# Optimization experiments

Hardware: AMD Instinct MI355X
Metric: run time of the kernel (lower is better)

The kernel has to match this reference:

```python
import jax, jax.numpy as jnp
import numpy as np

# module hyperparameters (from init_kwargs)
STRIDE, PAD, DIL = 1, 1, 1
GROUPS, DG = 1, 1
KH, KW = 3, 3
CIN, COUT = 256, 256


def _mdcn_forward(x, offset, mask, weight, bias):
    B, C, H, W = x.shape
    Cout = weight.shape[0]
    K = KH * KW
    Ho = (H + 2 * PAD - (DIL * (KH - 1) + 1)) // STRIDE + 1
    Wo = (W + 2 * PAD - (DIL * (KW - 1) + 1)) // STRIDE + 1
    Cg = C // DG

    # offset channel layout: ((g*K + k)*2 + {0: dy, 1: dx})
    off = offset.reshape(B, DG, KH, KW, 2, Ho, Wo)
    base_y = (jnp.arange(Ho) * STRIDE - PAD)[None, :] + DIL * jnp.arange(KH)[:, None]  # [KH,Ho]
    base_x = (jnp.arange(Wo) * STRIDE - PAD)[None, :] + DIL * jnp.arange(KW)[:, None]  # [KW,Wo]
    sy = base_y[None, None, :, None, :, None].astype(x.dtype) + off[:, :, :, :, 0]  # [B,DG,KH,KW,Ho,Wo]
    sx = base_x[None, None, None, :, None, :].astype(x.dtype) + off[:, :, :, :, 1]

    y0f = jnp.floor(sy); x0f = jnp.floor(sx)
    wy = sy - y0f; wx = sx - x0f
    y0 = y0f.astype(jnp.int32); x0 = x0f.astype(jnp.int32)

    xg = x.reshape(B, DG, Cg, H * W)

    def corner(yc, xc, w):
        valid = (yc >= 0) & (yc < H) & (xc >= 0) & (xc < W)
        idx = jnp.clip(yc, 0, H - 1) * W + jnp.clip(xc, 0, W - 1)  # [B,DG,KH,KW,Ho,Wo]
        v = jnp.take_along_axis(xg, idx.reshape(B, DG, 1, -1), axis=3)  # [B,DG,Cg,K*Ho*Wo]
        v = v.reshape(B, DG, Cg, KH, KW, Ho, Wo)
        return v * (w * valid.astype(x.dtype))[:, :, None]

    val = (corner(y0, x0, (1 - wy) * (1 - wx))
           + corner(y0, x0 + 1, (1 - wy) * wx)
           + corner(y0 + 1, x0, wy * (1 - wx))
           + corner(y0 + 1, x0 + 1, wy * wx))  # [B,DG,Cg,KH,KW,Ho,Wo]

    cols = val * mask.reshape(B, DG, 1, KH, KW, Ho, Wo)
    cols = cols.reshape(B, GROUPS, (C // GROUPS) * K, Ho * Wo)
    wg = weight.reshape(GROUPS, Cout // GROUPS, (C // GROUPS) * K)
    out = jnp.einsum('gok,bgkp->bgop', wg, cols).reshape(B, Cout, Ho, Wo)
    return out + bias[None, :, None, None]


def setup_inputs() -> dict:
    key = jax.random.key(0)
    k1, k2, k3, k4 = jax.random.split(key, 4)
    B, H, W = 4, 64, 64
    x = jax.random.normal(k1, (B, CIN, H, W), dtype=jnp.float32)
    offset = jax.random.normal(k2, (B, 2 * DG * KH * KW, H, W), dtype=jnp.float32)
    mask = jax.random.uniform(k3, (B, DG * KH * KW, H, W), dtype=jnp.float32)
    stdv = 1.0 / np.sqrt(CIN * KH * KW)
    weight = jax.random.uniform(k4, (COUT, CIN // GROUPS, KH, KW), dtype=jnp.float32,
                                minval=-stdv, maxval=stdv)
    bias = jnp.zeros((COUT,), dtype=jnp.float32)
    return {"x": x, "offset": offset, "mask": mask, "weight": weight, "bias": bias}


def reference(x, offset, mask, weight, bias):
    return _mdcn_forward(x, offset, mask, weight, bias)
```

## Files before the change

kernel.cpp:

```cpp
#include <hip/hip_runtime.h>
#include <hip/hip_bf16.h>
#include <stdint.h>

#define KDIM 2304

typedef __bf16 bf16_t;
typedef bf16_t bf16x8 __attribute__((ext_vector_type(8)));
typedef float f32x4 __attribute__((ext_vector_type(4)));
typedef float f32x2 __attribute__((ext_vector_type(2)));

__device__ __forceinline__ float b2f_lo(uint32_t u) {
  union { uint32_t i; float f; } c; c.i = u << 16; return c.f;
}
__device__ __forceinline__ float b2f_hi(uint32_t u) {
  union { uint32_t i; float f; } c; c.i = u & 0xffff0000u; return c.f;
}
__device__ __forceinline__ uint32_t pk_bf16(float a, float b) {
  __hip_bfloat162 h = __float22bfloat162_rn(make_float2(a, b));
  union { __hip_bfloat162 h; uint32_t u; } c; c.h = h; return c.u;
}

__global__ __launch_bounds__(256) void k_prep(const float* __restrict__ x,
                                              uint16_t* __restrict__ xt,
                                              const float* __restrict__ w,
                                              uint16_t* __restrict__ wt2) {
  int tid = threadIdx.x;
  if (blockIdx.x < 2048) {
    __shared__ float tile[32][65];
    int b = blockIdx.x >> 9;
    int cgrp = (blockIdx.x >> 6) & 7;
    int sgrp = blockIdx.x & 63;
    int c0 = cgrp << 5, s0 = sgrp << 6;
#pragma unroll
    for (int it = 0; it < 2; ++it) {
      int f = tid + it * 256;
      int rr = f >> 4, col = (f & 15) << 2;
      float4 v = *(const float4*)&x[((size_t)(b * 256 + c0 + rr)) * 4096 + s0 + col];
      tile[rr][col + 0] = v.x;
      tile[rr][col + 1] = v.y;
      tile[rr][col + 2] = v.z;
      tile[rr][col + 3] = v.w;
    }
    __syncthreads();
    int sp = tid >> 2, cg = tid & 3;
    uint4 o;
    o.x = pk_bf16(tile[cg * 8 + 0][sp], tile[cg * 8 + 1][sp]);
    o.y = pk_bf16(tile[cg * 8 + 2][sp], tile[cg * 8 + 3][sp]);
    o.z = pk_bf16(tile[cg * 8 + 4][sp], tile[cg * 8 + 5][sp]);
    o.w = pk_bf16(tile[cg * 8 + 6][sp], tile[cg * 8 + 7][sp]);
    *(uint4*)&xt[((size_t)b * 4096 + s0 + sp) * 256 + c0 + cg * 8] = o;
  } else {
    __shared__ float wl[2304];
    int row = blockIdx.x - 2048;
    const float* wrow = w + (size_t)row * KDIM;
    for (int i2 = tid; i2 < 2304; i2 += 256) wl[i2] = wrow[i2];
    __syncthreads();
    int strip = row >> 4, r16 = row & 15;
    for (int c = tid; c < 288; c += 256) {
      int tap = c >> 5, rem = c & 31;
      int w64 = rem >> 3, kh = (rem >> 2) & 1, seg = rem & 3;
      int i = tap * 4 + w64;
      int cin0 = w64 * 64 + kh * 32 + seg * 8;
      int lanex = seg * 16 + r16;
      uint16_t* dst = wt2 + (size_t)i * 16384 + (size_t)(strip * 128 + kh * 64 + lanex) * 8;
      uint4 o;
      o.x = pk_bf16(wl[(cin0 + 0) * 9 + tap], wl[(cin0 + 1) * 9 + tap]);
      o.y = pk_bf16(wl[(cin0 + 2) * 9 + tap], wl[(cin0 + 3) * 9 + tap]);
      o.z = pk_bf16(wl[(cin0 + 4) * 9 + tap], wl[(cin0 + 5) * 9 + tap]);
      o.w = pk_bf16(wl[(cin0 + 6) * 9 + tap], wl[(cin0 + 7) * 9 + tap]);
      *(uint4*)dst = o;
    }
  }
}

__device__ __forceinline__ void mk_corners(int tap, int p, int ho,
                                           const float* s_off, const float* s_msk,
                                           float cw[4], int cpo[4]) {
  int kh = tap / 3, kw = tap - kh * 3;
  float dy = s_off[(2 * tap) * 64 + p];
  float dx = s_off[(2 * tap + 1) * 64 + p];
  float mm = s_msk[tap * 64 + p];
  float sy = (float)(ho - 1 + kh) + dy;
  float sx = (float)(p - 1 + kw) + dx;
  float fy = floorf(sy), fx = floorf(sx);
  int y0 = (int)fy, x0 = (int)fx;
  float wy = sy - fy, wx = sx - fx;
#pragma unroll
  for (int cy = 0; cy < 2; ++cy) {
#pragma unroll
    for (int cx = 0; cx < 2; ++cx) {
      int y = y0 + cy, xx = x0 + cx;
      float wgt = (cy ? wy : 1.f - wy) * (cx ? wx : 1.f - wx) * mm;
      bool v = ((unsigned)y < 64u) && ((unsigned)xx < 64u);
      wgt = v ? wgt : 0.f;
      int yc = min(max(y, 0), 63), xc = min(max(xx, 0), 63);
      cw[cy * 2 + cx] = wgt;
      cpo[cy * 2 + cx] = ((yc << 6) + xc) * 256;
    }
  }
}

__global__ __launch_bounds__(512, 4) void k_fused(const uint16_t* __restrict__ xt,
                                                  const uint16_t* __restrict__ wt2,
                                                  const float* __restrict__ off,
                                                  const float* __restrict__ msk,
                                                  const float* __restrict__ bias,
                                                  float* __restrict__ out) {
  __shared__ __align__(16) uint16_t Bs[2][64][64];
  __shared__ float s_off[18 * 64];
  __shared__ float s_msk[9 * 64];

  int tid = threadIdx.x;
  int swz = ((int)blockIdx.x & 7) * 64 + ((int)blockIdx.x >> 3);
  int b = swz >> 7, ho = (swz >> 1) & 63, mh = swz & 1;

  const float* offb = off + (size_t)b * 18 * 4096 + ho * 64;
  for (int i = tid; i < 18 * 64; i += 512)
    s_off[i] = offb[(size_t)(i >> 6) * 4096 + (i & 63)];
  const float* mskb = msk + (size_t)b * 9 * 4096 + ho * 64;
  for (int i = tid; i < 9 * 64; i += 512)
    s_msk[i] = mskb[(size_t)(i >> 6) * 4096 + (i & 63)];

  int lane = tid & 63, wv = tid >> 6;
  int wm = wv >> 1, wn = wv & 1;
  int q = lane >> 4, r = lane & 15;
  int p = tid >> 3, cgh = tid & 7;
  const uint16_t* xtb = xt + (size_t)b * 1048576 + cgh * 8;
  int bcol = (cgh ^ (p & 7)) << 3;
  int awb = (mh * 4 + wm) * 2048;

  f32x4 acc[2][2];
#pragma unroll
  for (int mi = 0; mi < 2; ++mi)
#pragma unroll
    for (int ni = 0; ni < 2; ++ni) acc[mi][ni] = f32x4{0.f, 0.f, 0.f, 0.f};

  __syncthreads();

  float cw[4];
  int cpo[4];
  uint4 dnv[4];
  bf16x8 AFA[2][2], AFB[2][2];

  int c0 = (q ^ (r & 7)) << 3;
  int c1 = c0 ^ 32;
  int rb0 = (wn * 32 + r) * 64;

  mk_corners(0, p, ho, s_off, s_msk, cw, cpo);
#pragma unroll
  for (int c = 0; c < 4; ++c) dnv[c] = *(const uint4*)(xtb + cpo[c]);
  {
    const uint16_t* wp = wt2 + awb + lane * 8;
    AFA[0][0] = *(const bf16x8*)(wp);
    AFA[0][1] = *(const bf16x8*)(wp + 512);
    AFA[1][0] = *(const bf16x8*)(wp + 1024);
    AFA[1][1] = *(const bf16x8*)(wp + 1536);
  }
  {
    f32x2 f0 = {0.f, 0.f}, f1 = {0.f, 0.f}, f2 = {0.f, 0.f}, f3 = {0.f, 0.f};
#pragma unroll
    for (int c = 0; c < 4; ++c) {
      f32x2 wc = {cw[c], cw[c]};
      f0 += wc * f32x2{b2f_lo(dnv[c].x), b2f_hi(dnv[c].x)};
      f1 += wc * f32x2{b2f_lo(dnv[c].y), b2f_hi(dnv[c].y)};
      f2 += wc * f32x2{b2f_lo(dnv[c].z), b2f_hi(dnv[c].z)};
      f3 += wc * f32x2{b2f_lo(dnv[c].w), b2f_hi(dnv[c].w)};
    }
    uint4 o;
    o.x = pk_bf16(f0.x, f0.y);
    o.y = pk_bf16(f1.x, f1.y);
    o.z = pk_bf16(f2.x, f2.y);
    o.w = pk_bf16(f3.x, f3.y);
    *(uint4*)&Bs[0][p][bcol] = o;
  }
  __syncthreads();

#define BODY(I, AFC, AFN, DOMK, DODNV, DOAF, DOBL)                              \
  {                                                                             \
    if (DOMK) mk_corners(((I) + 1) >> 2, p, ho, s_off, s_msk, cw, cpo);         \
    if (DODNV) {                                                                \
      const int chw = (((I) + 1) & 3) << 6;                                     \
      dnv[0] = *(const uint4*)(xtb + cpo[0] + chw);                             \
      dnv[1] = *(const uint4*)(xtb + cpo[1] + chw);                             \
      dnv[2] = *(const uint4*)(xtb + cpo[2] + chw);                             \
      dnv[3] = *(const uint4*)(xtb + cpo[3] + chw);                             \
    }                                                                           \
    if (DOAF) {                                                                 \
      const uint16_t* wp = wt2 + (size_t)((I) + 1) * 16384 + awb + lane * 8;    \
      AFN[0][0] = *(const bf16x8*)(wp);                                         \
      AFN[0][1] = *(const bf16x8*)(wp + 512);                                   \
      AFN[1][0] = *(const bf16x8*)(wp + 1024);                                  \
      AFN[1][1] = *(const bf16x8*)(wp + 1536);                                  \
    }                                                                           \
    {                                                                           \
      const uint16_t* bsrow = &Bs[(I) & 1][0][0];                               \
      bf16x8 b00 = *(const bf16x8*)(bsrow + rb0 + c0);           \
      bf16x8 b01 = *(const bf16x8*)(bsrow + rb0 + c1);           \
      bf16x8 b10 = *(const bf16x8*)(bsrow + rb0 + 1024 + c0);    \
      bf16x8 b11 = *(const bf16x8*)(bsrow + rb0 + 1024 + c1);    \
      __builtin_amdgcn_s_setprio(1);                                            \
      acc[0][0] = __builtin_amdgcn_mfma_f32_16x16x32_bf16(AFC[0][0], b00, acc[0][0], 0, 0, 0); \
      acc[0][1] = __builtin_amdgcn_mfma_f32_16x16x32_bf16(AFC[0][0], b10, acc[0][1], 0, 0, 0); \
      acc[1][0] = __builtin_amdgcn_mfma_f32_16x16x32_bf16(AFC[1][0], b00, acc[1][0], 0, 0, 0); \
      acc[1][1] = __builtin_amdgcn_mfma_f32_16x16x32_bf16(AFC[1][0], b10, acc[1][1], 0, 0, 0); \
      acc[0][0] = __builtin_amdgcn_mfma_f32_16x16x32_bf16(AFC[0][1], b01, acc[0][0], 0, 0, 0); \
      acc[0][1] = __builtin_amdgcn_mfma_f32_16x16x32_bf16(AFC[0][1], b11, acc[0][1], 0, 0, 0); \
      acc[1][0] = __builtin_amdgcn_mfma_f32_16x16x32_bf16(AFC[1][1], b01, acc[1][0], 0, 0, 0); \
      acc[1][1] = __builtin_amdgcn_mfma_f32_16x16x32_bf16(AFC[1][1], b11, acc[1][1], 0, 0, 0); \
      __builtin_amdgcn_s_setprio(0);                                            \
    }                                                                           \
    if (DOBL) {                                                                 \
      f32x2 f0 = {0.f, 0.f}, f1 = {0.f, 0.f}, f2 = {0.f, 0.f}, f3 = {0.f, 0.f};\
      _Pragma("unroll")                                                         \
      for (int c = 0; c < 4; ++c) {                                             \
        f32x2 wc = {cw[c], cw[c]};                                              \
        f0 += wc * f32x2{b2f_lo(dnv[c].x), b2f_hi(dnv[c].x)};                   \
        f1 += wc * f32x2{b2f_lo(dnv[c].y), b2f_hi(dnv[c].y)};                   \
        f2 += wc * f32x2{b2f_lo(dnv[c].z), b2f_hi(dnv[c].z)};                   \
        f3 += wc * f32x2{b2f_lo(dnv[c].w), b2f_hi(dnv[c].w)};                   \
      }                                                                         \
      uint4 o;                                                                  \
      o.x = pk_bf16(f0.x, f0.y);                                                \
      o.y = pk_bf16(f1.x, f1.y);                                                \
      o.z = pk_bf16(f2.x, f2.y);                                                \
      o.w = pk_bf16(f3.x, f3.y);                                                \
      *(uint4*)&Bs[((I) + 1) & 1][p][bcol] = o;                                 \
    }                                                                           \
    __syncthreads();                                                            \
  }

#pragma unroll 1
  for (int ii = 0; ii < 8; ++ii) {
    int i0 = 4 * ii;
    BODY(i0 + 0, AFA, AFB, 0, 1, 1, 1)
    BODY(i0 + 1, AFB, AFA, 0, 1, 1, 1)
    BODY(i0 + 2, AFA, AFB, 0, 1, 1, 1)
    BODY(i0 + 3, AFB, AFA, 1, 1, 1, 1)
  }
  BODY(32, AFA, AFB, 0, 1, 1, 1)
  BODY(33, AFB, AFA, 0, 1, 1, 1)
  BODY(34, AFA, AFB, 0, 1, 1, 1)
  BODY(35, AFB, AFA, 0, 0, 0, 0)
#undef BODY

#pragma unroll
  for (int mi = 0; mi < 2; ++mi) {
#pragma unroll
    for (int j = 0; j < 4; ++j) {
      int m = mh * 128 + wm * 32 + mi * 16 + q * 4 + j;
      float bv = bias[m];
#pragma unroll
      for (int ni = 0; ni < 2; ++ni) {
        int wog = wn * 32 + ni * 16 + r;
        out[((size_t)(b * 256 + m)) * 4096 + ho * 64 + wog] = acc[mi][ni][j] + bv;
      }
    }
  }
}

extern "C" void kernel_launch(void* const* d_in, const int* in_sizes, int n_in,
                              void* d_out, int out_size, void* d_ws, size_t ws_size,
                              hipStream_t stream) {
  (void)in_sizes; (void)n_in; (void)out_size; (void)ws_size;
  const float* x      = (const float*)d_in[0];
  const float* offset = (const float*)d_in[1];
  const float* mask   = (const float*)d_in[2];
  const float* weight = (const float*)d_in[3];
  const float* bias   = (const float*)d_in[4];
  float* out = (float*)d_out;

  uint8_t* ws = (uint8_t*)d_ws;
  uint16_t* xt  = (uint16_t*)ws;
  uint16_t* wt2 = (uint16_t*)(ws + 8388608);

  k_prep<<<dim3(2304), 256, 0, stream>>>(x, xt, weight, wt2);
  k_fused<<<dim3(512), 512, 0, stream>>>(xt, wt2, offset, mask, bias, out);
}
```

Before: 128.5 us.

## Compute all 256 output channels per block and double the K step

Each block now covers the full 256-wide output-channel dimension with 1024 threads, instead of two blocks each covering half. The bilinear-sampled column tile is therefore gathered once per output row rather than twice. Each iteration now consumes 128 K-elements, which halves the iteration and barrier count. In exchange, weight fragments are loaded in the same iteration that uses them instead of being prefetched one step ahead, so global load latency is exposed before the MFMAs. The grid also shrinks to 256 large blocks, which limits occupancy options.

```diff
diff --git a/kernel.cpp b/kernel.cpp
--- a/kernel.cpp
+++ b/kernel.cpp
@@ -100,34 +100,34 @@
   }
 }
 
-__global__ __launch_bounds__(512, 4) void k_fused(const uint16_t* __restrict__ xt,
-                                                  const uint16_t* __restrict__ wt2,
-                                                  const float* __restrict__ off,
-                                                  const float* __restrict__ msk,
-                                                  const float* __restrict__ bias,
-                                                  float* __restrict__ out) {
-  __shared__ __align__(16) uint16_t Bs[2][64][64];
+__global__ __launch_bounds__(1024, 4) void k_fused(const uint16_t* __restrict__ xt,
+                                                   const uint16_t* __restrict__ wt2,
+                                                   const float* __restrict__ off,
+                                                   const float* __restrict__ msk,
+                                                   const float* __restrict__ bias,
+                                                   float* __restrict__ out) {
+  __shared__ __align__(16) uint16_t Bs[2][64][128];
   __shared__ float s_off[18 * 64];
   __shared__ float s_msk[9 * 64];
 
   int tid = threadIdx.x;
-  int swz = ((int)blockIdx.x & 7) * 64 + ((int)blockIdx.x >> 3);
-  int b = swz >> 7, ho = (swz >> 1) & 63, mh = swz & 1;
+  int swz = ((int)blockIdx.x & 7) * 32 + ((int)blockIdx.x >> 3);
+  int b = swz >> 6, ho = swz & 63;
 
   const float* offb = off + (size_t)b * 18 * 4096 + ho * 64;
-  for (int i = tid; i < 18 * 64; i += 512)
+  for (int i = tid; i < 18 * 64; i += 1024)
     s_off[i] = offb[(size_t)(i >> 6) * 4096 + (i & 63)];
   const float* mskb = msk + (size_t)b * 9 * 4096 + ho * 64;
-  for (int i = tid; i < 9 * 64; i += 512)
+  for (int i = tid; i < 9 * 64; i += 1024)
     s_msk[i] = mskb[(size_t)(i >> 6) * 4096 + (i & 63)];
 
   int lane = tid & 63, wv = tid >> 6;
   int wm = wv >> 1, wn = wv & 1;
   int q = lane >> 4, r = lane & 15;
-  int p = tid >> 3, cgh = tid & 7;
-  const uint16_t* xtb = xt + (size_t)b * 1048576 + cgh * 8;
-  int bcol = (cgh ^ (p & 7)) << 3;
-  int awb = (mh * 4 + wm) * 2048;
+  int p = tid >> 4, cg16 = tid & 15;
+  int half = cg16 >> 3, cg = cg16 & 7;
+  const uint16_t* xtb = xt + (size_t)b * 1048576 + cg * 8;
+  int wcol = (((half << 3) | (cg ^ (p & 7))) << 3);
 
   f32x4 acc[2][2];
 #pragma unroll
@@ -140,21 +140,17 @@
   float cw[4];
   int cpo[4];
   uint4 dnv[4];
-  bf16x8 AFA[2][2], AFB[2][2];
+  bf16x8 AF0[2][2], AF1[2][2];
 
   int c0 = (q ^ (r & 7)) << 3;
   int c1 = c0 ^ 32;
-  int rb0 = (wn * 32 + r) * 64;
+  int rowb0 = (wn * 32 + r) * 128;
 
   mk_corners(0, p, ho, s_off, s_msk, cw, cpo);
-#pragma unroll
-  for (int c = 0; c < 4; ++c) dnv[c] = *(const uint4*)(xtb + cpo[c]);
   {
-    const uint16_t* wp = wt2 + awb + lane * 8;
-    AFA[0][0] = *(const bf16x8*)(wp);
-    AFA[0][1] = *(const bf16x8*)(wp + 512);
-    AFA[1][0] = *(const bf16x8*)(wp + 1024);
-    AFA[1][1] = *(const bf16x8*)(wp + 1536);
+    const int chw = half << 6;
+#pragma unroll
+    for (int c = 0; c < 4; ++c) dnv[c] = *(const uint4*)(xtb + cpo[c] + chw);
   }
   {
     f32x2 f0 = {0.f, 0.f}, f1 = {0.f, 0.f}, f2 = {0.f, 0.f}, f3 = {0.f, 0.f};
@@ -171,42 +167,58 @@
     o.y = pk_bf16(f1.x, f1.y);
     o.z = pk_bf16(f2.x, f2.y);
     o.w = pk_bf16(f3.x, f3.y);
-    *(uint4*)&Bs[0][p][bcol] = o;
+    *(uint4*)&Bs[0][p][wcol] = o;
   }
   __syncthreads();
 
-#define BODY(I, AFC, AFN, DOMK, DODNV, DOAF, DOBL)                              \
+#define BODY(I, DOMK, DODNV, DOAF, DOBL)                                        \
   {                                                                             \
-    if (DOMK) mk_corners(((I) + 1) >> 2, p, ho, s_off, s_msk, cw, cpo);         \
+    if (DOMK) mk_corners(((I) + 1) >> 1, p, ho, s_off, s_msk, cw, cpo);         \
     if (DODNV) {                                                                \
-      const int chw = (((I) + 1) & 3) << 6;                                     \
+      const int chw = (((2 * ((I) + 1)) + half) & 3) << 6;                      \
       dnv[0] = *(const uint4*)(xtb + cpo[0] + chw);                             \
       dnv[1] = *(const uint4*)(xtb + cpo[1] + chw);                             \
       dnv[2] = *(const uint4*)(xtb + cpo[2] + chw);                             \
       dnv[3] = *(const uint4*)(xtb + cpo[3] + chw);                             \
     }                                                                           \
     if (DOAF) {                                                                 \
-      const uint16_t* wp = wt2 + (size_t)((I) + 1) * 16384 + awb + lane * 8;    \
-      AFN[0][0] = *(const bf16x8*)(wp);                                         \
-      AFN[0][1] = *(const bf16x8*)(wp + 512);                                   \
-      AFN[1][0] = *(const bf16x8*)(wp + 1024);                                  \
-      AFN[1][1] = *(const bf16x8*)(wp + 1536);                                  \
+      const uint16_t* wp = wt2 + (size_t)(2 * (I)) * 16384 + wm * 2048 + lane * 8; \
+      AF0[0][0] = *(const bf16x8*)(wp);                                         \
+      AF0[0][1] = *(const bf16x8*)(wp + 512);                                   \
+      AF0[1][0] = *(const bf16x8*)(wp + 1024);                                  \
+      AF0[1][1] = *(const bf16x8*)(wp + 1536);                                  \
+      AF1[0][0] = *(const bf16x8*)(wp + 16384);                                 \
+      AF1[0][1] = *(const bf16x8*)(wp + 16384 + 512);                           \
+      AF1[1][0] = *(const bf16x8*)(wp + 16384 + 1024);                          \
+      AF1[1][1] = *(const bf16x8*)(wp + 16384 + 1536);                          \
     }                                                                           \
     {                                                                           \
       const uint16_t* bsrow = &Bs[(I) & 1][0][0];                               \
-      bf16x8 b00 = *(const bf16x8*)(bsrow + rb0 + c0);           \
-      bf16x8 b01 = *(const bf16x8*)(bsrow + rb0 + c1);           \
-      bf16x8 b10 = *(const bf16x8*)(bsrow + rb0 + 1024 + c0);    \
-      bf16x8 b11 = *(const bf16x8*)(bsrow + rb0 + 1024 + c1);    \
+      bf16x8 bh0n0k0 = *(const bf16x8*)(bsrow + rowb0 + c0);                    \
+      bf16x8 bh0n0k1 = *(const bf16x8*)(bsrow + rowb0 + c1);                    \
+      bf16x8 bh0n1k0 = *(const bf16x8*)(bsrow + rowb0 + 2048 + c0);             \
+      bf16x8 bh0n1k1 = *(const bf16x8*)(bsrow + rowb0 + 2048 + c1);             \
+      bf16x8 bh1n0k0 = *(const bf16x8*)(bsrow + rowb0 + 64 + c0);               \
+      bf16x8 bh1n0k1 = *(const bf16x8*)(bsrow + rowb0 + 64 + c1);               \
+      bf16x8 bh1n1k0 = *(const bf16x8*)(bsrow + rowb0 + 2048 + 64 + c0);        \
+      bf16x8 bh1n1k1 = *(const bf16x8*)(bsrow + rowb0 + 2048 + 64 + c1);        \
       __builtin_amdgcn_s_setprio(1);                                            \
-      acc[0][0] = __builtin_amdgcn_mfma_f32_16x16x32_bf16(AFC[0][0], b00, acc[0][0], 0, 0, 0); \
-      acc[0][1] = __builtin_amdgcn_mfma_f32_16x16x32_bf16(AFC[0][0], b10, acc[0][1], 0, 0, 0); \
-      acc[1][0] = __builtin_amdgcn_mfma_f32_16x16x32_bf16(AFC[1][0], b00, acc[1][0], 0, 0, 0); \
-      acc[1][1] = __builtin_amdgcn_mfma_f32_16x16x32_bf16(AFC[1][0], b10, acc[1][1], 0, 0, 0); \
-      acc[0][0] = __builtin_amdgcn_mfma_f32_16x16x32_bf16(AFC[0][1], b01, acc[0][0], 0, 0, 0); \
-      acc[0][1] = __builtin_amdgcn_mfma_f32_16x16x32_bf16(AFC[0][1], b11, acc[0][1], 0, 0, 0); \
-      acc[1][0] = __builtin_amdgcn_mfma_f32_16x16x32_bf16(AFC[1][1], b01, acc[1][0], 0, 0, 0); \
-      acc[1][1] = __builtin_amdgcn_mfma_f32_16x16x32_bf16(AFC[1][1], b11, acc[1][1], 0, 0, 0); \
+      acc[0][0] = __builtin_amdgcn_mfma_f32_16x16x32_bf16(AF0[0][0], bh0n0k0, acc[0][0], 0, 0, 0); \
+      acc[0][1] = __builtin_amdgcn_mfma_f32_16x16x32_bf16(AF0[0][0], bh0n1k0, acc[0][1], 0, 0, 0); \
+      acc[1][0] = __builtin_amdgcn_mfma_f32_16x16x32_bf16(AF0[1][0], bh0n0k0, acc[1][0], 0, 0, 0); \
+      acc[1][1] = __builtin_amdgcn_mfma_f32_16x16x32_bf16(AF0[1][0], bh0n1k0, acc[1][1], 0, 0, 0); \
+      acc[0][0] = __builtin_amdgcn_mfma_f32_16x16x32_bf16(AF0[0][1], bh0n0k1, acc[0][0], 0, 0, 0); \
+      acc[0][1] = __builtin_amdgcn_mfma_f32_16x16x32_bf16(AF0[0][1], bh0n1k1, acc[0][1], 0, 0, 0); \
+      acc[1][0] = __builtin_amdgcn_mfma_f32_16x16x32_bf16(AF0[1][1], bh0n0k1, acc[1][0], 0, 0, 0); \
+      acc[1][1] = __builtin_amdgcn_mfma_f32_16x16x32_bf16(AF0[1][1], bh0n1k1, acc[1][1], 0, 0, 0); \
+      acc[0][0] = __builtin_amdgcn_mfma_f32_16x16x32_bf16(AF1[0][0], bh1n0k0, acc[0][0], 0, 0, 0); \
+      acc[0][1] = __builtin_amdgcn_mfma_f32_16x16x32_bf16(AF1[0][0], bh1n1k0, acc[0][1], 0, 0, 0); \
+      acc[1][0] = __builtin_amdgcn_mfma_f32_16x16x32_bf16(AF1[1][0], bh1n0k0, acc[1][0], 0, 0, 0); \
+      acc[1][1] = __builtin_amdgcn_mfma_f32_16x16x32_bf16(AF1[1][0], bh1n1k0, acc[1][1], 0, 0, 0); \
+      acc[0][0] = __builtin_amdgcn_mfma_f32_16x16x32_bf16(AF1[0][1], bh1n0k1, acc[0][0], 0, 0, 0); \
+      acc[0][1] = __builtin_amdgcn_mfma_f32_16x16x32_bf16(AF1[0][1], bh1n1k1, acc[0][1], 0, 0, 0); \
+      acc[1][0] = __builtin_amdgcn_mfma_f32_16x16x32_bf16(AF1[1][1], bh1n0k1, acc[1][0], 0, 0, 0); \
+      acc[1][1] = __builtin_amdgcn_mfma_f32_16x16x32_bf16(AF1[1][1], bh1n1k1, acc[1][1], 0, 0, 0); \
       __builtin_amdgcn_s_setprio(0);                                            \
     }                                                                           \
     if (DOBL) {                                                                 \
@@ -224,30 +236,25 @@
       o.y = pk_bf16(f1.x, f1.y);                                                \
       o.z = pk_bf16(f2.x, f2.y);                                                \
       o.w = pk_bf16(f3.x, f3.y);                                                \
-      *(uint4*)&Bs[((I) + 1) & 1][p][bcol] = o;                                 \
+      *(uint4*)&Bs[((I) + 1) & 1][p][wcol] = o;                                 \
     }                                                                           \
     __syncthreads();                                                            \
   }
 
 #pragma unroll 1
   for (int ii = 0; ii < 8; ++ii) {
-    int i0 = 4 * ii;
-    BODY(i0 + 0, AFA, AFB, 0, 1, 1, 1)
-    BODY(i0 + 1, AFB, AFA, 0, 1, 1, 1)
-    BODY(i0 + 2, AFA, AFB, 0, 1, 1, 1)
-    BODY(i0 + 3, AFB, AFA, 1, 1, 1, 1)
-  }
-  BODY(32, AFA, AFB, 0, 1, 1, 1)
-  BODY(33, AFB, AFA, 0, 1, 1, 1)
-  BODY(34, AFA, AFB, 0, 1, 1, 1)
-  BODY(35, AFB, AFA, 0, 0, 0, 0)
+    BODY(2 * ii + 0, 0, 1, 1, 1)
+    BODY(2 * ii + 1, 1, 1, 1, 1)
+  }
+  BODY(16, 0, 1, 1, 1)
+  BODY(17, 0, 0, 1, 0)
 #undef BODY
 
 #pragma unroll
   for (int mi = 0; mi < 2; ++mi) {
 #pragma unroll
     for (int j = 0; j < 4; ++j) {
-      int m = mh * 128 + wm * 32 + mi * 16 + q * 4 + j;
+      int m = wm * 32 + mi * 16 + q * 4 + j;
       float bv = bias[m];
 #pragma unroll
       for (int ni = 0; ni < 2; ++ni) {
@@ -274,5 +281,5 @@
   uint16_t* wt2 = (uint16_t*)(ws + 8388608);
 
   k_prep<<<dim3(2304), 256, 0, stream>>>(x, xt, weight, wt2);
-  k_fused<<<dim3(512), 512, 0, stream>>>(xt, wt2, offset, mask, bias, out);
-}
+  k_fused<<<dim3(256), 1024, 0, stream>>>(xt, wt2, offset, mask, bias, out);
+}
```

New measurement: 124.3 us. 1.03x faster.
